# Kernel tuning notes

Measured on AMD Instinct MI355X. Metric: run time of the kernel, lower is better.

Reference implementation:

```python
import jax, jax.numpy as jnp
import numpy as np

N_NODES = 50000
N_EDGES = 300000
N_ETYPES = 4
D = 256          # input_dim == output_dim (no zero-pad branch in GatedGraphConv)
RES = 768        # res_feature_dim
N_GRAPHS = 128
N_STEPS = 8
HID = 256        # classifier hidden dim


def setup_inputs() -> dict:
    key = jax.random.key(0)
    ks = jax.random.split(key, 12)
    s = 0.05
    return {
        "features": jax.random.normal(ks[0], (N_NODES, D + RES), jnp.float32),
        "W_e": jax.random.normal(ks[1], (N_ETYPES, D, D), jnp.float32) * s,
        "b_e": jnp.zeros((N_ETYPES, D), jnp.float32),
        "W_ih": jax.random.normal(ks[2], (D, 3 * D), jnp.float32) * s,
        "W_hh": jax.random.normal(ks[3], (D, 3 * D), jnp.float32) * s,
        "b_ih": jnp.zeros((3 * D,), jnp.float32),
        "b_hh": jnp.zeros((3 * D,), jnp.float32),
        "W1": jax.random.normal(ks[4], (D + RES, HID), jnp.float32) * s,
        "b1": jnp.zeros((HID,), jnp.float32),
        "W2": jax.random.normal(ks[5], (HID, 1), jnp.float32) * s,
        "b2": jnp.zeros((1,), jnp.float32),
        "src": jax.random.randint(ks[6], (N_EDGES,), 0, N_NODES),
        "dst": jax.random.randint(ks[7], (N_EDGES,), 0, N_NODES),
        "etypes": jax.random.randint(ks[8], (N_EDGES,), 0, N_ETYPES),
        "node2graph": jnp.sort(jax.random.randint(ks[9], (N_NODES,), 0, N_GRAPHS)),
    }


def _gru_cell(x, h, W_ih, W_hh, b_ih, b_hh):
    # PyTorch GRUCell, gate order (r, z, n)
    gi = x @ W_ih + b_ih
    gh = h @ W_hh + b_hh
    i_r, i_z, i_n = jnp.split(gi, 3, axis=-1)
    h_r, h_z, h_n = jnp.split(gh, 3, axis=-1)
    r = jax.nn.sigmoid(i_r + h_r)
    z = jax.nn.sigmoid(i_z + h_z)
    n = jnp.tanh(i_n + r * h_n)
    return (1.0 - z) * n + z * h


def reference(features, W_e, b_e, W_ih, W_hh, b_ih, b_hh, W1, b1, W2, b2,
              src, dst, etypes, node2graph):
    h = features[:, :D]          # node features fed to GGNN
    res = features[:, D:]        # mixed residual features (bypass GGNN)

    def step(h, _):
        # per-edge-type linear on all nodes: [T, N, D]
        ht = jnp.einsum('nd,tde->tne', h, W_e) + b_e[:, None, :]
        msgs = ht[etypes, src]                                   # [E, D]
        a = jax.ops.segment_sum(msgs, dst, num_segments=N_NODES)  # scatter-add to dst
        return _gru_cell(a, h, W_ih, W_hh, b_ih, b_hh), None

    h, _ = jax.lax.scan(step, h, None, length=N_STEPS)

    out = jnp.concatenate([h, res], axis=1)  # [N, D+RES]
    # masked mean over nodes of each graph == segment mean
    sums = jax.ops.segment_sum(out, node2graph, num_segments=N_GRAPHS)
    cnts = jax.ops.segment_sum(jnp.ones((N_NODES,), out.dtype), node2graph,
                               num_segments=N_GRAPHS)
    pooled = sums / jnp.maximum(cnts, 1.0)[:, None]  # [B, D+RES]

    # classifier (dropouts inactive at eval): Linear -> ReLU -> Linear -> sigmoid
    hcls = jax.nn.relu(pooled @ W1 + b1)
    logits = hcls @ W2 + b2
    return jax.nn.sigmoid(logits)  # [B, 1]
```

## Files before the change

kernel.cpp:

```cpp
#include <hip/hip_runtime.h>
#include <math.h>
#include <stdint.h>

#define NN 50000
#define NE 300000
#define NG 128
#define NSTEP 8
#define MPAD 50048
#define SCB 196
#define PCH 8

#define BM 128
#define BN 128
#define BK 64

typedef __attribute__((ext_vector_type(8))) short bf16x8;
typedef __attribute__((ext_vector_type(4))) float f32x4;
typedef unsigned short u16;
typedef unsigned int u32;

__device__ __forceinline__ float b2f(u16 u) {
  union { u32 i; float f; } c; c.i = ((u32)u) << 16; return c.f;
}
__device__ __forceinline__ u16 f2b(float f) {
  union { float f; u32 i; } c; c.f = f;
  u32 x = c.i;
  u32 r = (x + 0x7fffu + ((x >> 16) & 1u)) >> 16;
  return (u16)r;
}

__device__ __forceinline__ void load_lds16(const void* g, void* l) {
  __builtin_amdgcn_global_load_lds((const __attribute__((address_space(1))) u32*)g,
                                   (__attribute__((address_space(3))) u32*)l, 16, 0, 0);
}

__global__ void k_conv_we(const float* __restrict__ W_e, u16* __restrict__ Wt) {
  int i = blockIdx.x * 256 + threadIdx.x;
  int c = i >> 8, d = i & 255;
  Wt[c * 256 + d] = f2b(W_e[(c >> 8) * 65536 + d * 256 + (c & 255)]);
}
__global__ void k_conv_rz(const float* __restrict__ W_ih, const float* __restrict__ W_hh,
                          u16* __restrict__ ah, u16* __restrict__ ha) {
  int i = blockIdx.x * 256 + threadIdx.x;
  int n = i >> 9, k = i & 511;
  float va = (k < 256) ? W_ih[k * 768 + n] : W_hh[(k - 256) * 768 + n];
  float vh = (k < 256) ? W_hh[k * 768 + n] : W_ih[(k - 256) * 768 + n];
  ah[n * 512 + k] = f2b(va);
  ha[n * 512 + k] = f2b(vh);
}
__global__ void k_conv_n(const float* __restrict__ W, u16* __restrict__ Wt) {
  int i = blockIdx.x * 256 + threadIdx.x;
  int n = i >> 8, k = i & 255;
  Wt[n * 256 + k] = f2b(W[k * 768 + 512 + n]);
}
__global__ void k_brz(const float* __restrict__ b_ih, const float* __restrict__ b_hh,
                      float* __restrict__ b_rz) {
  int i = blockIdx.x * 256 + threadIdx.x;
  if (i < 512) b_rz[i] = b_ih[i] + b_hh[i];
}

__global__ void k_init_h(const float* __restrict__ feat, u16* __restrict__ acat) {
  int i = blockIdx.x * 256 + threadIdx.x;
  int n = i >> 6, d = (i & 63) << 2;
  ushort4 o;
  if (n < NN) {
    float4 v = *(const float4*)(feat + (size_t)n * 1024 + d);
    o.x = f2b(v.x); o.y = f2b(v.y); o.z = f2b(v.z); o.w = f2b(v.w);
  } else {
    o.x = o.y = o.z = o.w = 0;
  }
  *(ushort4*)(acat + (size_t)n * 768 + d) = o;
}

__global__ void k_hist(const int* __restrict__ dst, int* __restrict__ deg) {
  int e = blockIdx.x * 256 + threadIdx.x;
  if (e < NE) atomicAdd(&deg[dst[e]], 1);
}
__global__ void k_scan1(const int* __restrict__ deg, int* __restrict__ part, int* __restrict__ bsum) {
  __shared__ int sh[256];
  int b = blockIdx.x, t = threadIdx.x;
  int i = b * 256 + t;
  int v = (i < NN) ? deg[i] : 0;
  sh[t] = v;
  __syncthreads();
  for (int off = 1; off < 256; off <<= 1) {
    int tmp = (t >= off) ? sh[t - off] : 0;
    __syncthreads();
    sh[t] += tmp;
    __syncthreads();
  }
  if (i < NN) part[i] = sh[t] - v;
  if (t == 255) bsum[b] = sh[255];
}
__global__ void k_scan2(const int* __restrict__ bsum, int* __restrict__ boff) {
  __shared__ int sh[256];
  int t = threadIdx.x;
  int v = (t < SCB) ? bsum[t] : 0;
  sh[t] = v;
  __syncthreads();
  for (int off = 1; off < 256; off <<= 1) {
    int tmp = (t >= off) ? sh[t - off] : 0;
    __syncthreads();
    sh[t] += tmp;
    __syncthreads();
  }
  boff[t] = sh[t] - v;
  if (t == 255) boff[256] = sh[255];
}
__global__ void k_scan3(const int* __restrict__ part, const int* __restrict__ boff, int* __restrict__ rp) {
  int i = blockIdx.x * 256 + threadIdx.x;
  if (i < NN) rp[i] = part[i] + boff[i >> 8];
  if (i == NN) rp[NN] = boff[256];
}
__global__ void k_scatter(const int* __restrict__ src, const int* __restrict__ dst,
                          const int* __restrict__ ety, const int* __restrict__ rp,
                          int* __restrict__ cursor, int* __restrict__ goff) {
  int e = blockIdx.x * 256 + threadIdx.x;
  if (e < NE) {
    int d = dst[e];
    int p = rp[d] + atomicAdd(&cursor[d], 1);
    goff[p] = src[e] * 1024 + ety[e] * 256;
  }
}
__global__ void k_gstart(const int* __restrict__ n2g, int* __restrict__ gstart) {
  int n = blockIdx.x * 256 + threadIdx.x;
  if (n >= NN) return;
  int g = n2g[n];
  int gp = (n == 0) ? -1 : n2g[n - 1];
  for (int x = gp + 1; x <= g; ++x) gstart[x] = n;
  if (n == NN - 1)
    for (int x = g + 1; x <= NG; ++x) gstart[x] = NN;
}

template <int MODE>
__global__ __launch_bounds__(256, 2) void k_gemm(const u16* __restrict__ A, int lda, int K,
                                                 const u16* __restrict__ Bt,
                                                 const float* __restrict__ bias,
                                                 u16* __restrict__ C, int ldc,
                                                 const u16* __restrict__ rzb,
                                                 const u16* __restrict__ inb,
                                                 const u16* __restrict__ hold,
                                                 u16* __restrict__ hnew) {
  __shared__ __align__(16) char lds[(BM + BN) * BK * 2];
  char* As = lds;
  char* Bs = lds + BM * BK * 2;
  const int tid = threadIdx.x;
  const int w = tid >> 6, l = tid & 63;
  const int m0 = blockIdx.y * BM, n0 = blockIdx.x * BN;
  const int rld = tid >> 3;
  const int cld = tid & 7;
  const int wm = (w >> 1) * 64, wn = (w & 1) * 64;
  const int fr = l & 15, kq = l >> 4;
  f32x4 acc[4][4];
#pragma unroll
  for (int m = 0; m < 4; ++m)
#pragma unroll
    for (int n = 0; n < 4; ++n) acc[m][n] = (f32x4){0.f, 0.f, 0.f, 0.f};

  for (int k0 = 0; k0 < K; k0 += BK) {
#pragma unroll
    for (int p = 0; p < 4; ++p) {
      int row = p * 32 + rld;
      int ks = k0 + ((cld ^ (row & 7)) << 3);
      load_lds16(A + (size_t)(m0 + row) * lda + ks, As + p * 4096 + w * 1024);
    }
#pragma unroll
    for (int p = 0; p < 4; ++p) {
      int row = p * 32 + rld;
      int ks = k0 + ((cld ^ (row & 7)) << 3);
      load_lds16(Bt + (size_t)(n0 + row) * K + ks, Bs + p * 4096 + w * 1024);
    }
    asm volatile("s_waitcnt vmcnt(0)" ::: "memory");
    __syncthreads();
#pragma unroll
    for (int kk = 0; kk < BK; kk += 32) {
      bf16x8 af[4], bfr[4];
      int kb = (kk + kq * 8) * 2;
#pragma unroll
      for (int m = 0; m < 4; ++m) {
        int R = wm + m * 16 + fr;
        af[m] = *(const bf16x8*)(As + R * 128 + (kb ^ ((R & 7) << 4)));
      }
#pragma unroll
      for (int n = 0; n < 4; ++n) {
        int R = wn + n * 16 + fr;
        bfr[n] = *(const bf16x8*)(Bs + R * 128 + (kb ^ ((R & 7) << 4)));
      }
#pragma unroll
      for (int m = 0; m < 4; ++m)
#pragma unroll
        for (int n = 0; n < 4; ++n)
          acc[m][n] = __builtin_amdgcn_mfma_f32_16x16x32_bf16(af[m], bfr[n], acc[m][n], 0, 0, 0);
    }
    __syncthreads();
  }
#pragma unroll
  for (int m = 0; m < 4; ++m) {
#pragma unroll
    for (int n = 0; n < 4; ++n) {
      int col = n0 + wn + n * 16 + fr;
      float bv = bias[col];
#pragma unroll
      for (int j = 0; j < 4; ++j) {
        int row = m0 + wm + m * 16 + kq * 4 + j;
        float v = acc[m][n][j] + bv;
        if (MODE == 0) {
          C[(size_t)row * ldc + col] = f2b(v);
        } else if (MODE == 1) {
          C[(size_t)row * ldc + col] = f2b(1.f / (1.f + expf(-v)));
        } else {
          float r = b2f(rzb[(size_t)row * 512 + col]);
          float z = b2f(rzb[(size_t)row * 512 + 256 + col]);
          float in_ = b2f(inb[(size_t)row * 256 + col]);
          float ho = b2f(hold[(size_t)row * 768 + col]);
          float ng = tanhf(in_ + r * v);
          float hv = (1.f - z) * ng + z * ho;
          hnew[(size_t)row * 768 + col] = f2b(hv);
        }
      }
    }
  }
}

__global__ __launch_bounds__(256) void k_aggr(const u16* __restrict__ ht, const int* __restrict__ rp,
                                              const int* __restrict__ goff, u16* __restrict__ acat) {
  int w = threadIdx.x >> 6, l = threadIdx.x & 63;
  int n = blockIdx.x * 4 + w;
  if (n >= MPAD) return;
  float a0 = 0.f, a1 = 0.f, a2 = 0.f, a3 = 0.f;
  if (n < NN) {
    int s = rp[n], e = rp[n + 1];
    for (int i = s; i < e; ++i) {
      const u16* pm = ht + (size_t)goff[i] + l * 4;
      ushort4 u = *(const ushort4*)pm;
      a0 += b2f(u.x); a1 += b2f(u.y); a2 += b2f(u.z); a3 += b2f(u.w);
    }
  }
  ushort4 o;
  o.x = f2b(a0); o.y = f2b(a1); o.z = f2b(a2); o.w = f2b(a3);
  *(ushort4*)(acat + (size_t)n * 768 + 256 + l * 4) = o;
}

__global__ __launch_bounds__(256) void k_pool(const u16* __restrict__ hb, const float* __restrict__ feat,
                                              const int* __restrict__ gstart, float* __restrict__ pooled) {
  int g = blockIdx.x, ch = blockIdx.y, t = threadIdx.x;
  int s = gstart[g], e = gstart[g + 1];
  int tot = e - s;
  int per = (tot + PCH - 1) / PCH;
  int ns = s + ch * per;
  int ne = ns + per < e ? ns + per : e;
  if (ns >= ne) return;
  int c = t << 2;
  float a0 = 0.f, a1 = 0.f, a2 = 0.f, a3 = 0.f;
  if (c < 256) {
    for (int n = ns; n < ne; ++n) {
      ushort4 u = *(const ushort4*)(hb + (size_t)n * 768 + c);
      a0 += b2f(u.x); a1 += b2f(u.y); a2 += b2f(u.z); a3 += b2f(u.w);
    }
  } else {
    for (int n = ns; n < ne; ++n) {
      float4 v = *(const float4*)(feat + (size_t)n * 1024 + c);
      a0 += v.x; a1 += v.y; a2 += v.z; a3 += v.w;
    }
  }
  atomicAdd(&pooled[g * 1024 + c], a0);
  atomicAdd(&pooled[g * 1024 + c + 1], a1);
  atomicAdd(&pooled[g * 1024 + c + 2], a2);
  atomicAdd(&pooled[g * 1024 + c + 3], a3);
}

__global__ __launch_bounds__(256) void k_head(const float* __restrict__ pooled,
                                              const int* __restrict__ gstart,
                                              const float* __restrict__ W1, const float* __restrict__ b1,
                                              const float* __restrict__ W2, const float* __restrict__ b2,
                                              float* __restrict__ out) {
  __shared__ float sp[1024];
  __shared__ float red[256];
  int g = blockIdx.x, t = threadIdx.x;
  float inv = 1.f / fmaxf((float)(gstart[g + 1] - gstart[g]), 1.f);
  for (int i = t; i < 1024; i += 256) sp[i] = pooled[g * 1024 + i] * inv;
  __syncthreads();
  float acc = b1[t];
  for (int k = 0; k < 1024; ++k) acc += sp[k] * W1[k * 256 + t];
  float hc = fmaxf(acc, 0.f);
  red[t] = hc * W2[t];
  __syncthreads();
  for (int s2 = 128; s2 > 0; s2 >>= 1) {
    if (t < s2) red[t] += red[t + s2];
    __syncthreads();
  }
  if (t == 0) out[g] = 1.f / (1.f + expf(-(red[0] + b2[0])));
}

extern "C" void kernel_launch(void* const* d_in, const int* in_sizes, int n_in, void* d_out, int out_size,
                              void* d_ws, size_t ws_size, hipStream_t stream) {
  const float* feat = (const float*)d_in[0];
  const float* W_e = (const float*)d_in[1];
  const float* b_e = (const float*)d_in[2];
  const float* W_ih = (const float*)d_in[3];
  const float* W_hh = (const float*)d_in[4];
  const float* b_ih = (const float*)d_in[5];
  const float* b_hh = (const float*)d_in[6];
  const float* W1 = (const float*)d_in[7];
  const float* b1 = (const float*)d_in[8];
  const float* W2 = (const float*)d_in[9];
  const float* b2 = (const float*)d_in[10];
  const int* src = (const int*)d_in[11];
  const int* dst = (const int*)d_in[12];
  const int* ety = (const int*)d_in[13];
  const int* n2g = (const int*)d_in[14];

  char* p = (char*)d_ws;
  auto alloc = [&](size_t b) { char* r = p; p += (b + 255) & ~(size_t)255; return r; };
  u16* acat = (u16*)alloc((size_t)MPAD * 768 * 2);
  u16* ht = (u16*)alloc((size_t)MPAD * 1024 * 2);
  u16* rzb = (u16*)alloc((size_t)MPAD * 512 * 2);
  u16* inb = (u16*)alloc((size_t)MPAD * 256 * 2);
  u16* Wt_e = (u16*)alloc(1024 * 256 * 2);
  u16* Wt_rz_ah = (u16*)alloc(512 * 512 * 2);
  u16* Wt_rz_ha = (u16*)alloc(512 * 512 * 2);
  u16* Wt_in = (u16*)alloc(256 * 256 * 2);
  u16* Wt_hn = (u16*)alloc(256 * 256 * 2);
  float* b_rz = (float*)alloc(512 * 4);
  int* deg = (int*)alloc((size_t)NN * 4);
  int* part = (int*)alloc((size_t)NN * 4);
  int* bsum = (int*)alloc(SCB * 4);
  int* boff = (int*)alloc(257 * 4);
  int* rp = (int*)alloc((size_t)(NN + 1) * 4);
  int* cursor = (int*)alloc((size_t)NN * 4);
  int* goff = (int*)alloc((size_t)NE * 4);
  int* gstart = (int*)alloc((size_t)(NG + 1) * 4);
  float* pooled = (float*)alloc((size_t)NG * 1024 * 4);

  hipMemsetAsync(deg, 0, (size_t)NN * 4, stream);
  hipMemsetAsync(cursor, 0, (size_t)NN * 4, stream);
  hipMemsetAsync(pooled, 0, (size_t)NG * 1024 * 4, stream);

  k_conv_we<<<1024, 256, 0, stream>>>(W_e, Wt_e);
  k_conv_rz<<<1024, 256, 0, stream>>>(W_ih, W_hh, Wt_rz_ah, Wt_rz_ha);
  k_conv_n<<<256, 256, 0, stream>>>(W_ih, Wt_in);
  k_conv_n<<<256, 256, 0, stream>>>(W_hh, Wt_hn);
  k_brz<<<2, 256, 0, stream>>>(b_ih, b_hh, b_rz);
  k_init_h<<<MPAD / 4, 256, 0, stream>>>(feat, acat);
  k_hist<<<(NE + 255) / 256, 256, 0, stream>>>(dst, deg);
  k_scan1<<<SCB, 256, 0, stream>>>(deg, part, bsum);
  k_scan2<<<1, 256, 0, stream>>>(bsum, boff);
  k_scan3<<<SCB + 1, 256, 0, stream>>>(part, boff, rp);
  k_scatter<<<(NE + 255) / 256, 256, 0, stream>>>(src, dst, ety, rp, cursor, goff);
  k_gstart<<<SCB, 256, 0, stream>>>(n2g, gstart);

  for (int s = 0; s < NSTEP; ++s) {
    int hboff = (s & 1) ? 512 : 0;
    int hnewoff = 512 - hboff;
    int rzoff = (s & 1) ? 256 : 0;
    const u16* Wrz = (s & 1) ? Wt_rz_ah : Wt_rz_ha;
    k_gemm<0><<<dim3(1024 / BN, MPAD / BM), 256, 0, stream>>>(
        acat + hboff, 768, 256, Wt_e, b_e, ht, 1024, nullptr, nullptr, nullptr, nullptr);
    k_aggr<<<MPAD / 4, 256, 0, stream>>>(ht, rp, goff, acat);
    k_gemm<1><<<dim3(512 / BN, MPAD / BM), 256, 0, stream>>>(
        acat + rzoff, 768, 512, Wrz, b_rz, rzb, 512, nullptr, nullptr, nullptr, nullptr);
    k_gemm<0><<<dim3(256 / BN, MPAD / BM), 256, 0, stream>>>(
        acat + 256, 768, 256, Wt_in, b_ih + 512, inb, 256, nullptr, nullptr, nullptr, nullptr);
    k_gemm<2><<<dim3(256 / BN, MPAD / BM), 256, 0, stream>>>(
        acat + hboff, 768, 256, Wt_hn, b_hh + 512, nullptr, 0, rzb, inb, acat + hboff,
        acat + hnewoff);
  }

  k_pool<<<dim3(NG, PCH), 256, 0, stream>>>(acat, feat, gstart, pooled);
  k_head<<<NG, 256, 0, stream>>>(pooled, gstart, W1, b1, W2, b2, (float*)d_out);
}
```

Measured before the change: 1.858 ms.

## Aggregate-then-transform per edge type, fusing message GEMM and input-gate GEMM

Reorders the message computation so source features are first summed per (destination, edge type) segment, then multiplied by the per-type weight. This avoids materializing the full per-type transformed node tensor (four times the feature width) every step. The edge bias is added as count times bias. The aggregated result is kept in LDS and reused for the input-side n-gate GEMM in the same kernel, dropping one separate GEMM launch. In exchange, the gather runs inside a GEMM kernel with irregular per-row loop lengths, which may cause load imbalance. The CSR build is also expanded to per-type segments.

Measured after the change: 2.216 ms. 1.19x slower.

```diff
diff --git a/kernel.cpp b/kernel.cpp
--- a/kernel.cpp
+++ b/kernel.cpp
@@ -4,17 +4,21 @@
 
 #define NN 50000
 #define NE 300000
+#define NT4 200000
 #define NG 128
 #define NSTEP 8
 #define MPAD 50048
 #define SCB 196
+#define SCB2 782
 #define PCH 8
+#define EM 64
 
 #define BM 128
 #define BN 128
 #define BK 64
 
 typedef __attribute__((ext_vector_type(8))) short bf16x8;
+typedef __attribute__((ext_vector_type(8))) unsigned short u16x8;
 typedef __attribute__((ext_vector_type(4))) float f32x4;
 typedef unsigned short u16;
 typedef unsigned int u32;
@@ -72,15 +76,16 @@
   *(ushort4*)(acat + (size_t)n * 768 + d) = o;
 }
 
-__global__ void k_hist(const int* __restrict__ dst, int* __restrict__ deg) {
+__global__ void k_hist(const int* __restrict__ dst, const int* __restrict__ ety,
+                       int* __restrict__ deg2) {
   int e = blockIdx.x * 256 + threadIdx.x;
-  if (e < NE) atomicAdd(&deg[dst[e]], 1);
-}
-__global__ void k_scan1(const int* __restrict__ deg, int* __restrict__ part, int* __restrict__ bsum) {
+  if (e < NE) atomicAdd(&deg2[dst[e] * 4 + ety[e]], 1);
+}
+__global__ void k_scan1(const int* __restrict__ deg2, int* __restrict__ part, int* __restrict__ bsum) {
   __shared__ int sh[256];
   int b = blockIdx.x, t = threadIdx.x;
   int i = b * 256 + t;
-  int v = (i < NN) ? deg[i] : 0;
+  int v = (i < NT4) ? deg2[i] : 0;
   sh[t] = v;
   __syncthreads();
   for (int off = 1; off < 256; off <<= 1) {
@@ -89,38 +94,50 @@
     sh[t] += tmp;
     __syncthreads();
   }
-  if (i < NN) part[i] = sh[t] - v;
+  if (i < NT4) part[i] = sh[t] - v;
   if (t == 255) bsum[b] = sh[255];
 }
 __global__ void k_scan2(const int* __restrict__ bsum, int* __restrict__ boff) {
-  __shared__ int sh[256];
+  __shared__ int sh[1024];
   int t = threadIdx.x;
-  int v = (t < SCB) ? bsum[t] : 0;
+  int v = (t < SCB2) ? bsum[t] : 0;
   sh[t] = v;
   __syncthreads();
-  for (int off = 1; off < 256; off <<= 1) {
+  for (int off = 1; off < 1024; off <<= 1) {
     int tmp = (t >= off) ? sh[t - off] : 0;
     __syncthreads();
     sh[t] += tmp;
     __syncthreads();
   }
   boff[t] = sh[t] - v;
-  if (t == 255) boff[256] = sh[255];
-}
-__global__ void k_scan3(const int* __restrict__ part, const int* __restrict__ boff, int* __restrict__ rp) {
+  if (t == 1023) boff[1024] = sh[1023];
+}
+__global__ void k_scan3(const int* __restrict__ part, const int* __restrict__ boff, int* __restrict__ rp2) {
   int i = blockIdx.x * 256 + threadIdx.x;
-  if (i < NN) rp[i] = part[i] + boff[i >> 8];
-  if (i == NN) rp[NN] = boff[256];
+  if (i < NT4) rp2[i] = part[i] + boff[i >> 8];
+  if (i == NT4) rp2[NT4] = boff[1024];
 }
 __global__ void k_scatter(const int* __restrict__ src, const int* __restrict__ dst,
-                          const int* __restrict__ ety, const int* __restrict__ rp,
-                          int* __restrict__ cursor, int* __restrict__ goff) {
+                          const int* __restrict__ ety, const int* __restrict__ rp2,
+                          int* __restrict__ cursor2, int* __restrict__ esrc) {
   int e = blockIdx.x * 256 + threadIdx.x;
   if (e < NE) {
-    int d = dst[e];
-    int p = rp[d] + atomicAdd(&cursor[d], 1);
-    goff[p] = src[e] * 1024 + ety[e] * 256;
-  }
+    int seg = dst[e] * 4 + ety[e];
+    int p = rp2[seg] + atomicAdd(&cursor2[seg], 1);
+    esrc[p] = src[e];
+  }
+}
+__global__ void k_cnt2(const int* __restrict__ deg2, ushort4* __restrict__ cnt2) {
+  int v = blockIdx.x * 256 + threadIdx.x;
+  if (v >= MPAD) return;
+  ushort4 o;
+  if (v < NN) {
+    o.x = (u16)deg2[v * 4 + 0]; o.y = (u16)deg2[v * 4 + 1];
+    o.z = (u16)deg2[v * 4 + 2]; o.w = (u16)deg2[v * 4 + 3];
+  } else {
+    o.x = o.y = o.z = o.w = 0;
+  }
+  cnt2[v] = o;
 }
 __global__ void k_gstart(const int* __restrict__ n2g, int* __restrict__ gstart) {
   int n = blockIdx.x * 256 + threadIdx.x;
@@ -130,6 +147,160 @@
   for (int x = gp + 1; x <= g; ++x) gstart[x] = n;
   if (n == NN - 1)
     for (int x = g + 1; x <= NG; ++x) gstart[x] = NN;
+}
+
+__global__ __launch_bounds__(256, 2) void k_eagg(
+    const u16* __restrict__ acat, int hboff,
+    const int* __restrict__ rp2, const int* __restrict__ esrc,
+    const u16* __restrict__ Wt_e, const u16* __restrict__ Wt_in,
+    const ushort4* __restrict__ cnt2, const float* __restrict__ b_e,
+    const float* __restrict__ b_ih512,
+    u16* __restrict__ acat_out, u16* __restrict__ inb) {
+  __shared__ __align__(16) char Ss[EM * 512];
+  __shared__ __align__(16) char Bs[256 * 128];
+  const int tid = threadIdx.x;
+  const int w = tid >> 6, l = tid & 63;
+  const int m0 = blockIdx.x * EM;
+  const int fr = l & 15, kq = l >> 4;
+  const int wn = w * 64;
+  const int rld = tid >> 3, cld = tid & 7;
+  const int h2 = l >> 5, lw = l & 31;
+  f32x4 acc[4][4];
+#pragma unroll
+  for (int m = 0; m < 4; ++m)
+#pragma unroll
+    for (int n = 0; n < 4; ++n) acc[m][n] = (f32x4){0.f, 0.f, 0.f, 0.f};
+
+  for (int t = 0; t < 4; ++t) {
+    if (t > 0) __syncthreads();
+    for (int r8 = 0; r8 < 8; ++r8) {
+      int row = w * 16 + (h2 << 3) + r8;
+      int v = m0 + row;
+      int s = 0, e = 0;
+      if (v < NN) { s = rp2[v * 4 + t]; e = rp2[v * 4 + t + 1]; }
+      float g0 = 0, g1 = 0, g2 = 0, g3 = 0, g4 = 0, g5 = 0, g6 = 0, g7 = 0;
+      for (int i = s; i < e; ++i) {
+        const u16* hp = acat + (size_t)esrc[i] * 768 + hboff + lw * 8;
+        u16x8 u = *(const u16x8*)hp;
+        g0 += b2f(u[0]); g1 += b2f(u[1]); g2 += b2f(u[2]); g3 += b2f(u[3]);
+        g4 += b2f(u[4]); g5 += b2f(u[5]); g6 += b2f(u[6]); g7 += b2f(u[7]);
+      }
+      u16x8 o;
+      o[0] = f2b(g0); o[1] = f2b(g1); o[2] = f2b(g2); o[3] = f2b(g3);
+      o[4] = f2b(g4); o[5] = f2b(g5); o[6] = f2b(g6); o[7] = f2b(g7);
+      *(u16x8*)(Ss + row * 512 + ((lw * 16) ^ ((row & 7) << 4))) = o;
+    }
+    const u16* Bw = Wt_e + (size_t)t * 65536;
+    for (int kc = 0; kc < 4; ++kc) {
+      __syncthreads();
+#pragma unroll
+      for (int p = 0; p < 8; ++p) {
+        int brow = p * 32 + rld;
+        int ks = kc * 64 + ((cld ^ (brow & 7)) << 3);
+        load_lds16(Bw + (size_t)brow * 256 + ks, Bs + p * 4096 + w * 1024);
+      }
+      asm volatile("s_waitcnt vmcnt(0)" ::: "memory");
+      __syncthreads();
+#pragma unroll
+      for (int kk = 0; kk < 64; kk += 32) {
+        bf16x8 af[4], bfr[4];
+        int kb = (kk + kq * 8) * 2;
+        int ka = (kc * 64 + kk + kq * 8) * 2;
+#pragma unroll
+        for (int m = 0; m < 4; ++m) {
+          int R = m * 16 + fr;
+          af[m] = *(const bf16x8*)(Ss + R * 512 + (ka ^ ((R & 7) << 4)));
+        }
+#pragma unroll
+        for (int n = 0; n < 4; ++n) {
+          int R = wn + n * 16 + fr;
+          bfr[n] = *(const bf16x8*)(Bs + R * 128 + (kb ^ ((R & 7) << 4)));
+        }
+#pragma unroll
+        for (int m = 0; m < 4; ++m)
+#pragma unroll
+          for (int n = 0; n < 4; ++n)
+            acc[m][n] = __builtin_amdgcn_mfma_f32_16x16x32_bf16(af[m], bfr[n], acc[m][n], 0, 0, 0);
+      }
+    }
+  }
+  __syncthreads();
+
+  float bev[4][4];
+#pragma unroll
+  for (int n = 0; n < 4; ++n)
+#pragma unroll
+    for (int t = 0; t < 4; ++t) bev[n][t] = b_e[t * 256 + wn + n * 16 + fr];
+#pragma unroll
+  for (int m = 0; m < 4; ++m) {
+#pragma unroll
+    for (int j = 0; j < 4; ++j) {
+      int r = m * 16 + kq * 4 + j;
+      int v = m0 + r;
+      ushort4 c4 = cnt2[v];
+      float c0 = c4.x, c1 = c4.y, c2 = c4.z, c3 = c4.w;
+#pragma unroll
+      for (int n = 0; n < 4; ++n) {
+        int col = wn + n * 16 + fr;
+        float val = acc[m][n][j] + c0 * bev[n][0] + c1 * bev[n][1] + c2 * bev[n][2] + c3 * bev[n][3];
+        u16 vb = f2b(val);
+        acat_out[(size_t)v * 768 + 256 + col] = vb;
+        *(u16*)(Ss + r * 512 + ((col * 2) ^ ((r & 7) << 4))) = vb;
+      }
+    }
+  }
+#pragma unroll
+  for (int m = 0; m < 4; ++m)
+#pragma unroll
+    for (int n = 0; n < 4; ++n) acc[m][n] = (f32x4){0.f, 0.f, 0.f, 0.f};
+
+  for (int kc = 0; kc < 4; ++kc) {
+    __syncthreads();
+#pragma unroll
+    for (int p = 0; p < 8; ++p) {
+      int brow = p * 32 + rld;
+      int ks = kc * 64 + ((cld ^ (brow & 7)) << 3);
+      load_lds16(Wt_in + (size_t)brow * 256 + ks, Bs + p * 4096 + w * 1024);
+    }
+    asm volatile("s_waitcnt vmcnt(0)" ::: "memory");
+    __syncthreads();
+#pragma unroll
+    for (int kk = 0; kk < 64; kk += 32) {
+      bf16x8 af[4], bfr[4];
+      int kb = (kk + kq * 8) * 2;
+      int ka = (kc * 64 + kk + kq * 8) * 2;
+#pragma unroll
+      for (int m = 0; m < 4; ++m) {
+        int R = m * 16 + fr;
+        af[m] = *(const bf16x8*)(Ss + R * 512 + (ka ^ ((R & 7) << 4)));
+      }
+#pragma unroll
+      for (int n = 0; n < 4; ++n) {
+        int R = wn + n * 16 + fr;
+        bfr[n] = *(const bf16x8*)(Bs + R * 128 + (kb ^ ((R & 7) << 4)));
+      }
+#pragma unroll
+      for (int m = 0; m < 4; ++m)
+#pragma unroll
+        for (int n = 0; n < 4; ++n)
+          acc[m][n] = __builtin_amdgcn_mfma_f32_16x16x32_bf16(af[m], bfr[n], acc[m][n], 0, 0, 0);
+    }
+  }
+  float bi[4];
+#pragma unroll
+  for (int n = 0; n < 4; ++n) bi[n] = b_ih512[wn + n * 16 + fr];
+#pragma unroll
+  for (int m = 0; m < 4; ++m) {
+#pragma unroll
+    for (int j = 0; j < 4; ++j) {
+      int v = m0 + m * 16 + kq * 4 + j;
+#pragma unroll
+      for (int n = 0; n < 4; ++n) {
+        int col = wn + n * 16 + fr;
+        inb[(size_t)v * 256 + col] = f2b(acc[m][n][j] + bi[n]);
+      }
+    }
+  }
 }
 
 template <int MODE>
@@ -204,9 +375,7 @@
       for (int j = 0; j < 4; ++j) {
         int row = m0 + wm + m * 16 + kq * 4 + j;
         float v = acc[m][n][j] + bv;
-        if (MODE == 0) {
-          C[(size_t)row * ldc + col] = f2b(v);
-        } else if (MODE == 1) {
+        if (MODE == 1) {
           C[(size_t)row * ldc + col] = f2b(1.f / (1.f + expf(-v)));
         } else {
           float r = b2f(rzb[(size_t)row * 512 + col]);
@@ -220,25 +389,6 @@
       }
     }
   }
-}
-
-__global__ __launch_bounds__(256) void k_aggr(const u16* __restrict__ ht, const int* __restrict__ rp,
-                                              const int* __restrict__ goff, u16* __restrict__ acat) {
-  int w = threadIdx.x >> 6, l = threadIdx.x & 63;
-  int n = blockIdx.x * 4 + w;
-  if (n >= MPAD) return;
-  float a0 = 0.f, a1 = 0.f, a2 = 0.f, a3 = 0.f;
-  if (n < NN) {
-    int s = rp[n], e = rp[n + 1];
-    for (int i = s; i < e; ++i) {
-      const u16* pm = ht + (size_t)goff[i] + l * 4;
-      ushort4 u = *(const ushort4*)pm;
-      a0 += b2f(u.x); a1 += b2f(u.y); a2 += b2f(u.z); a3 += b2f(u.w);
-    }
-  }
-  ushort4 o;
-  o.x = f2b(a0); o.y = f2b(a1); o.z = f2b(a2); o.w = f2b(a3);
-  *(ushort4*)(acat + (size_t)n * 768 + 256 + l * 4) = o;
 }
 
 __global__ __launch_bounds__(256) void k_pool(const u16* __restrict__ hb, const float* __restrict__ feat,
@@ -313,7 +463,6 @@
   char* p = (char*)d_ws;
   auto alloc = [&](size_t b) { char* r = p; p += (b + 255) & ~(size_t)255; return r; };
   u16* acat = (u16*)alloc((size_t)MPAD * 768 * 2);
-  u16* ht = (u16*)alloc((size_t)MPAD * 1024 * 2);
   u16* rzb = (u16*)alloc((size_t)MPAD * 512 * 2);
   u16* inb = (u16*)alloc((size_t)MPAD * 256 * 2);
   u16* Wt_e = (u16*)alloc(1024 * 256 * 2);
@@ -322,18 +471,19 @@
   u16* Wt_in = (u16*)alloc(256 * 256 * 2);
   u16* Wt_hn = (u16*)alloc(256 * 256 * 2);
   float* b_rz = (float*)alloc(512 * 4);
-  int* deg = (int*)alloc((size_t)NN * 4);
-  int* part = (int*)alloc((size_t)NN * 4);
-  int* bsum = (int*)alloc(SCB * 4);
-  int* boff = (int*)alloc(257 * 4);
-  int* rp = (int*)alloc((size_t)(NN + 1) * 4);
-  int* cursor = (int*)alloc((size_t)NN * 4);
-  int* goff = (int*)alloc((size_t)NE * 4);
+  int* deg2 = (int*)alloc((size_t)NT4 * 4);
+  int* part = (int*)alloc((size_t)NT4 * 4);
+  int* bsum = (int*)alloc((size_t)SCB2 * 4);
+  int* boff = (int*)alloc(1025 * 4);
+  int* rp2 = (int*)alloc((size_t)(NT4 + 1) * 4);
+  int* cursor2 = (int*)alloc((size_t)NT4 * 4);
+  int* esrc = (int*)alloc((size_t)NE * 4);
+  ushort4* cnt2 = (ushort4*)alloc((size_t)MPAD * 8);
   int* gstart = (int*)alloc((size_t)(NG + 1) * 4);
   float* pooled = (float*)alloc((size_t)NG * 1024 * 4);
 
-  hipMemsetAsync(deg, 0, (size_t)NN * 4, stream);
-  hipMemsetAsync(cursor, 0, (size_t)NN * 4, stream);
+  hipMemsetAsync(deg2, 0, (size_t)NT4 * 4, stream);
+  hipMemsetAsync(cursor2, 0, (size_t)NT4 * 4, stream);
   hipMemsetAsync(pooled, 0, (size_t)NG * 1024 * 4, stream);
 
   k_conv_we<<<1024, 256, 0, stream>>>(W_e, Wt_e);
@@ -342,11 +492,12 @@
   k_conv_n<<<256, 256, 0, stream>>>(W_hh, Wt_hn);
   k_brz<<<2, 256, 0, stream>>>(b_ih, b_hh, b_rz);
   k_init_h<<<MPAD / 4, 256, 0, stream>>>(feat, acat);
-  k_hist<<<(NE + 255) / 256, 256, 0, stream>>>(dst, deg);
-  k_scan1<<<SCB, 256, 0, stream>>>(deg, part, bsum);
-  k_scan2<<<1, 256, 0, stream>>>(bsum, boff);
-  k_scan3<<<SCB + 1, 256, 0, stream>>>(part, boff, rp);
-  k_scatter<<<(NE + 255) / 256, 256, 0, stream>>>(src, dst, ety, rp, cursor, goff);
+  k_hist<<<(NE + 255) / 256, 256, 0, stream>>>(dst, ety, deg2);
+  k_scan1<<<SCB2, 256, 0, stream>>>(deg2, part, bsum);
+  k_scan2<<<1, 1024, 0, stream>>>(bsum, boff);
+  k_scan3<<<SCB2 + 1, 256, 0, stream>>>(part, boff, rp2);
+  k_scatter<<<(NE + 255) / 256, 256, 0, stream>>>(src, dst, ety, rp2, cursor2, esrc);
+  k_cnt2<<<(MPAD + 255) / 256, 256, 0, stream>>>(deg2, cnt2);
   k_gstart<<<SCB, 256, 0, stream>>>(n2g, gstart);
 
   for (int s = 0; s < NSTEP; ++s) {
@@ -354,13 +505,10 @@
     int hnewoff = 512 - hboff;
     int rzoff = (s & 1) ? 256 : 0;
     const u16* Wrz = (s & 1) ? Wt_rz_ah : Wt_rz_ha;
-    k_gemm<0><<<dim3(1024 / BN, MPAD / BM), 256, 0, stream>>>(
-        acat + hboff, 768, 256, Wt_e, b_e, ht, 1024, nullptr, nullptr, nullptr, nullptr);
-    k_aggr<<<MPAD / 4, 256, 0, stream>>>(ht, rp, goff, acat);
+    k_eagg<<<MPAD / EM, 256, 0, stream>>>(acat, hboff, rp2, esrc, Wt_e, Wt_in, cnt2, b_e,
+                                          b_ih + 512, acat, inb);
     k_gemm<1><<<dim3(512 / BN, MPAD / BM), 256, 0, stream>>>(
         acat + rzoff, 768, 512, Wrz, b_rz, rzb, 512, nullptr, nullptr, nullptr, nullptr);
-    k_gemm<0><<<dim3(256 / BN, MPAD / BM), 256, 0, stream>>>(
-        acat + 256, 768, 256, Wt_in, b_ih + 512, inb, 256, nullptr, nullptr, nullptr, nullptr);
     k_gemm<2><<<dim3(256 / BN, MPAD / BM), 256, 0, stream>>>(
         acat + hboff, 768, 256, Wt_hn, b_hh + 512, nullptr, 0, rzb, inb, acat + hboff,
         acat + hnewoff);
```
